# Kernel optimization log

Hardware: AMD Instinct MI355X
Metric: run time of the kernel (lower is better)

The kernel has to match this reference:

```python
import jax, jax.numpy as jnp
import numpy as np

B, S, D, H = 2, 2048, 1024, 16
HD = D // H  # 64
EPS = 1e-6


def setup_inputs() -> dict:
    key = jax.random.key(0)
    ks = jax.random.split(key, 12)
    s = 1.0 / np.sqrt(D)
    return {
        "query": jax.random.normal(ks[0], (B, S, D), jnp.float32),
        "key": jax.random.normal(ks[1], (B, S, D), jnp.float32),
        "value": jax.random.normal(ks[2], (B, S, D), jnp.float32),
        "mask": jax.random.randint(ks[3], (B, S, S), 0, 2) == 1,
        "Wq": jax.random.normal(ks[4], (D, D), jnp.float32) * s,
        "bq": jnp.zeros((D,), jnp.float32),
        "Wk": jax.random.normal(ks[5], (D, D), jnp.float32) * s,
        "bk": jnp.zeros((D,), jnp.float32),
        "Wv": jax.random.normal(ks[6], (D, D), jnp.float32) * s,
        "bv": jnp.zeros((D,), jnp.float32),
        "Wo": jax.random.normal(ks[7], (D, D), jnp.float32) * s,
        "bo": jnp.zeros((D,), jnp.float32),
        "gamma": jnp.ones((D,), jnp.float32),
        "beta": jnp.zeros((D,), jnp.float32),
    }


def reference(query, key, value, mask, Wq, bq, Wk, bk, Wv, bv, Wo, bo, gamma, beta):
    b, sq, _ = query.shape
    sk = key.shape[1]
    # QKV projections -> [b, h, s, hd]
    q = (query @ Wq + bq).reshape(b, sq, H, HD).transpose(0, 2, 1, 3)
    k = (key @ Wk + bk).reshape(b, sk, H, HD).transpose(0, 2, 1, 3)
    v = (value @ Wv + bv).reshape(b, sk, H, HD).transpose(0, 2, 1, 3)
    # scores [b, h, sq, sk]
    scores = jnp.einsum("bhqd,bhkd->bhqk", q, k) / jnp.sqrt(jnp.float32(HD))
    scores = jnp.where(mask[:, None, :, :], -jnp.inf, scores)
    attn = jax.nn.softmax(scores, axis=-1)  # dropout: eval mode (identity)
    out = jnp.einsum("bhqk,bhkd->bhqd", attn, v)
    out = out.transpose(0, 2, 1, 3).reshape(b, sq, H * HD)
    out = out @ Wo + bo
    # residual + LayerNorm with unbiased std and (std + eps) denominator (faithful to torch code)
    x = query + out
    mean = x.mean(-1, keepdims=True)
    std = jnp.std(x, axis=-1, keepdims=True, ddof=1)
    return gamma * (x - mean) / (std + EPS) + beta
```

## Files before the change

### kernel.cpp

```cpp
#include <hip/hip_runtime.h>


#define NB 2
#define SS 2048
#define DDIM 1024
#define NH 16
#define HDIM 64
#define MROWS (NB * SS)

typedef unsigned short u16;
typedef unsigned long long u64;
typedef unsigned int u32;
typedef short bf16x8 __attribute__((ext_vector_type(8)));
typedef float f32x4 __attribute__((ext_vector_type(4)));

typedef const __attribute__((address_space(1))) void GASV;
typedef __attribute__((address_space(3))) void LASV;

__device__ __forceinline__ float dev_exp2(float x) {
  float r;
  asm("v_exp_f32 %0, %1" : "=v"(r) : "v"(x));
  return r;
}

__device__ __forceinline__ u16 f2bf(float f) {
  unsigned u = __builtin_bit_cast(unsigned, f);
  u += 0x7FFFu + ((u >> 16) & 1u);
  return (u16)(u >> 16);
}

__device__ __forceinline__ u32 cvt_pk_bf16(float a, float b) {
  u32 d;
  asm("v_cvt_pk_bf16_f32 %0, %1, %2" : "=v"(d) : "v"(a), "v"(b));
  return d;
}

__global__ __launch_bounds__(256) void cvt_bf16_3(const float* __restrict__ q,
                                                  const float* __restrict__ k,
                                                  const float* __restrict__ v,
                                                  u16* __restrict__ out) {
  const float* in = (blockIdx.y == 0) ? q : (blockIdx.y == 1) ? k : v;
  size_t i = ((size_t)blockIdx.x * 256 + threadIdx.x) * 4;
  float4 val = *(const float4*)(in + i);
  uint2 o;
  u16* po = (u16*)&o;
  po[0] = f2bf(val.x); po[1] = f2bf(val.y); po[2] = f2bf(val.z); po[3] = f2bf(val.w);
  *(uint2*)(out + (size_t)blockIdx.y * MROWS * DDIM + i) = o;
}

__global__ __launch_bounds__(256) void cvt_mask_bits(const int* __restrict__ in,
                                                     u64* __restrict__ out) {
  size_t w = ((size_t)blockIdx.x * 256 + threadIdx.x) >> 6;
  int lane = threadIdx.x & 63;
  int v = in[w * 64 + lane];
  u64 bits = __ballot(v != 0);
  if (lane == 0) out[w] = bits;
}

__global__ __launch_bounds__(256) void transpose_cvt_w4(const float* __restrict__ W0,
                                                        const float* __restrict__ W1,
                                                        const float* __restrict__ W2,
                                                        const float* __restrict__ W3,
                                                        u16* __restrict__ WTbase) {
  __shared__ u16 t[64][65];
  const int z = blockIdx.z;
  const float* W = (z == 0) ? W0 : (z == 1) ? W1 : (z == 2) ? W2 : W3;
  u16* WT = WTbase + (size_t)z * DDIM * DDIM;
  const int k0 = blockIdx.x * 64, n0 = blockIdx.y * 64;
  const int tid = threadIdx.x;
  const int r = tid >> 4;
  const int c4 = (tid & 15) * 4;
#pragma unroll
  for (int it = 0; it < 4; ++it) {
    int k = r + it * 16;
    float4 v = *(const float4*)&W[(size_t)(k0 + k) * DDIM + n0 + c4];
    t[c4 + 0][k] = f2bf(v.x);
    t[c4 + 1][k] = f2bf(v.y);
    t[c4 + 2][k] = f2bf(v.z);
    t[c4 + 3][k] = f2bf(v.w);
  }
  __syncthreads();
#pragma unroll
  for (int it = 0; it < 4; ++it) {
    int n = r + it * 16;
    uint2 o;
    u16* po = (u16*)&o;
#pragma unroll
    for (int j = 0; j < 4; ++j) po[j] = t[n][c4 + j];
    *(uint2*)&WT[(size_t)(n0 + n) * DDIM + k0 + c4] = o;
  }
}

template <int MODE>
__global__ __launch_bounds__(256) void gemm_bt(const u16* __restrict__ Abase,
                                               const u16* __restrict__ BT,
                                               const float* __restrict__ b0,
                                               const float* __restrict__ b1,
                                               const float* __restrict__ b2,
                                               const float* __restrict__ resid,
                                               void* __restrict__ C,
                                               void* __restrict__ Cv) {
  __shared__ __align__(16) u16 SMEM[2][2][128][64];
  u16(&Al)[2][128][64] = SMEM[0];
  u16(&Bl)[2][128][64] = SMEM[1];
  const int tid = threadIdx.x;
  const int wid = tid >> 6, lane = tid & 63;
  const int wm = (wid >> 1) * 64, wn = (wid & 1) * 64;
  const int nwg = gridDim.x * gridDim.y;
  const int lin = blockIdx.y * 32 + blockIdx.x;
  const int wg = (lin & 7) * (nwg >> 3) + (lin >> 3);
  const int rowA0 = (wg & 31) * 128, colB0 = (wg >> 5) * 128;
  const int sel = (MODE == 0) ? (colB0 >> 10) : 0;
  const u16* Ag = Abase + (size_t)sel * ((size_t)MROWS * DDIM) + (size_t)rowA0 * DDIM;
  const u16* Bg = BT + (size_t)colB0 * DDIM;
  f32x4 acc[4][4] = {};
  const int rl = lane >> 3;
  const int ce = (lane & 7) * 8;

#define G_STAGE(buf, kt)                                                       \
  do {                                                                         \
    _Pragma("unroll") for (int c = 0; c < 4; ++c) {                            \
      int rt = wid * 32 + c * 8;                                               \
      __builtin_amdgcn_global_load_lds(                                        \
          (GASV*)(Ag + (size_t)(rt + rl) * DDIM + (kt) + ce),                  \
          (LASV*)((char*)&Al[buf][0][0] + rt * 128), 16, 0, 0);                \
      __builtin_amdgcn_global_load_lds(                                        \
          (GASV*)(Bg + (size_t)(rt + rl) * DDIM + (kt) + ce),                  \
          (LASV*)((char*)&Bl[buf][0][0] + rt * 128), 16, 0, 0);                \
    }                                                                          \
  } while (0)

  G_STAGE(0, 0);
  __syncthreads();
  for (int t = 0; t < 16; ++t) {
    const int cur = t & 1;
    if (t < 15) G_STAGE(cur ^ 1, (t + 1) * 64);
#pragma unroll
    for (int kk = 0; kk < 64; kk += 32) {
      bf16x8 af[4], bfr[4];
#pragma unroll
      for (int i = 0; i < 4; ++i)
        af[i] = *(const bf16x8*)&Al[cur][wm + i * 16 + (lane & 15)][kk + (lane >> 4) * 8];
#pragma unroll
      for (int j = 0; j < 4; ++j)
        bfr[j] = *(const bf16x8*)&Bl[cur][wn + j * 16 + (lane & 15)][kk + (lane >> 4) * 8];
#pragma unroll
      for (int i = 0; i < 4; ++i)
#pragma unroll
        for (int j = 0; j < 4; ++j)
          acc[i][j] = __builtin_amdgcn_mfma_f32_16x16x32_bf16(af[i], bfr[j], acc[i][j], 0, 0, 0);
    }
    __syncthreads();
  }
#undef G_STAGE

  const int cb = lane & 15, hi = lane >> 4;
  if (MODE == 0) {
    if (sel == 2) {
      u16(*T)[136] = (u16(*)[136]) & SMEM[0][0][0][0];
      const int dcol0 = colB0 & 1023;
#pragma unroll
      for (int j = 0; j < 4; ++j) {
        int dl = wn + j * 16 + cb;
        float bv = b2[dcol0 + dl];
#pragma unroll
        for (int i = 0; i < 4; ++i) {
          int sl = wm + i * 16 + hi * 4;
          uint2 o;
          o.x = cvt_pk_bf16(acc[i][j][0] + bv, acc[i][j][1] + bv);
          o.y = cvt_pk_bf16(acc[i][j][2] + bv, acc[i][j][3] + bv);
          *(uint2*)&T[dl][sl] = o;
        }
      }
      __syncthreads();
      const int bb = rowA0 >> 11, s0 = rowA0 & (SS - 1);
#pragma unroll
      for (int it = 0; it < 8; ++it) {
        int chunk = it * 256 + tid;
        int dl = chunk >> 4;
        int sc = (chunk & 15) * 8;
        int dg = dcol0 + dl;
        *(bf16x8*)&((u16*)Cv)[((size_t)(bb * NH + (dg >> 6)) * HDIM + (dg & 63)) * SS +
                              s0 + sc] = *(const bf16x8*)&T[dl][sc];
      }
    } else {
      const float* bp = (sel == 0) ? b0 : b1;
      const float scale = (sel == 0) ? 0.125f * 1.44269504088896340736f : 1.0f;
      u16* dst = (u16*)C + (size_t)sel * ((size_t)MROWS * DDIM);
      const int colw0 = (colB0 & 1023) + wn;
#pragma unroll
      for (int i = 0; i < 4; ++i)
#pragma unroll
        for (int j = 0; j < 4; ++j) {
          int colw = colw0 + j * 16 + cb;
          float bv = bp[colw];
#pragma unroll
          for (int r = 0; r < 4; ++r) {
            int row = rowA0 + wm + i * 16 + hi * 4 + r;
            dst[(size_t)row * DDIM + colw] = f2bf((acc[i][j][r] + bv) * scale);
          }
        }
    }
  } else {
#pragma unroll
    for (int i = 0; i < 4; ++i)
#pragma unroll
      for (int j = 0; j < 4; ++j) {
        int col = colB0 + wn + j * 16 + cb;
        float bv = b0[col];
#pragma unroll
        for (int r = 0; r < 4; ++r) {
          int row = rowA0 + wm + i * 16 + hi * 4 + r;
          size_t off = (size_t)row * DDIM + col;
          ((float*)C)[off] = acc[i][j][r] + bv + resid[off];
        }
      }
  }
}

__global__ __launch_bounds__(256, 4) void attn_fwd(const u16* __restrict__ Qp,
                                                   const u16* __restrict__ Kp,
                                                   const u16* __restrict__ VpT,
                                                   const u64* __restrict__ Mbits,
                                                   u16* __restrict__ O) {
  __shared__ __align__(16) u16 Kl[2][64][64];
  __shared__ __align__(16) u16 Vl[2][64][64];
  __shared__ __align__(16) u16 Pl[4][16][64];
  const int tid = threadIdx.x, wid = tid >> 6, lane = tid & 63;
  const int bid = blockIdx.x;
  const int bh = (bid & 7) * 4 + ((bid >> 3) & 3);
  const int q0 = (bid >> 5) * 64;
  const int b = bh >> 4, h = bh & 15;
  const int hi = lane >> 4, cbase = lane & 15, lx = lane & 7;

  bf16x8 qf[2];
  {
    const u16* qb = Qp + (size_t)(b * SS + q0 + wid * 16 + cbase) * DDIM + h * 64 + hi * 8;
    qf[0] = *(const bf16x8*)qb;
    qf[1] = *(const bf16x8*)(qb + 32);
  }
  float l_run = 0.f;
  f32x4 accO[4];
#pragma unroll
  for (int f = 0; f < 4; ++f) accO[f] = (f32x4){0.f, 0.f, 0.f, 0.f};

  const u16* Kgb = Kp + (size_t)b * SS * DDIM + h * 64;
  const u16* Vgb = VpT + (size_t)bh * 64 * SS;
  const u64* Mb = Mbits + (size_t)(b * SS + q0 + wid * 16 + cbase) * (SS / 64);
  const int rl = lane >> 3;
  const int ceS = ((lane & 7) ^ rl) * 8;

  int fo[4][2];
#pragma unroll
  for (int f = 0; f < 4; ++f)
#pragma unroll
    for (int ks = 0; ks < 2; ++ks)
      fo[f][ks] = (f * 16 + cbase) * 64 + (((ks * 4 + hi) ^ lx) << 3);
  int pw[4];
#pragma unroll
  for (int f = 0; f < 4; ++f)
    pw[f] = cbase * 64 + (((f * 2 + (hi >> 1)) ^ lx) << 3) + ((hi & 1) << 2);
  u16* KlF = &Kl[0][0][0];
  u16* VlF = &Vl[0][0][0];
  u16* Plw = &Pl[wid][0][0];

#define STAGE_KV(BUF, kv)                                                      \
  do {                                                                         \
    _Pragma("unroll") for (int c = 0; c < 2; ++c) {                            \
      int rt = wid * 16 + c * 8;                                               \
      __builtin_amdgcn_global_load_lds(                                        \
          (GASV*)(Kgb + (size_t)((kv) + rt + rl) * DDIM + ceS),                \
          (LASV*)((char*)KlF + (BUF) * 8192 + rt * 128), 16, 0, 0);            \
      __builtin_amdgcn_global_load_lds(                                        \
          (GASV*)(Vgb + (size_t)(rt + rl) * SS + (kv) + ceS),                  \
          (LASV*)((char*)VlF + (BUF) * 8192 + rt * 128), 16, 0, 0);            \
    }                                                                          \
  } while (0)

#define ATTN_ITER(T, CUR, DO_STAGE, MROW)                                      \
  do {                                                                         \
    if (DO_STAGE) STAGE_KV((CUR) ^ 1, ((T) + 1) * 64);                         \
    f32x4 sc[4];                                                               \
    __builtin_amdgcn_s_setprio(1);                                             \
    _Pragma("unroll") for (int fn = 0; fn < 4; ++fn) {                         \
      f32x4 c = (f32x4){0.f, 0.f, 0.f, 0.f};                                   \
      _Pragma("unroll") for (int ks = 0; ks < 2; ++ks) {                       \
        bf16x8 kf = *(const bf16x8*)(KlF + (CUR) * 4096 + fo[fn][ks]);         \
        c = __builtin_amdgcn_mfma_f32_16x16x32_bf16(kf, qf[ks], c, 0, 0, 0);   \
      }                                                                        \
      sc[fn] = c;                                                              \
    }                                                                          \
    __builtin_amdgcn_s_setprio(0);                                             \
             \
    u64 mh = (MROW) >> (hi * 4);                                               \
    u32 mlo = (u32)mh, mhi2 = (u32)(mh >> 32);                                 \
    float rs0 = 0.f, rs1 = 0.f;                                                \
    _Pragma("unroll") for (int fn = 0; fn < 4; ++fn) {                         \
      u32 b4 = ((fn < 2) ? mlo : mhi2) >> ((fn & 1) * 16);                     \
      _Pragma("unroll") for (int j = 0; j < 4; ++j) {                          \
        float bf_ = (float)((b4 >> j) & 1u);                                   \
        float p = dev_exp2(fmaf(bf_, -512.f, sc[fn][j]));                      \
        sc[fn][j] = p;                                                         \
        if (j & 1) rs1 += p; else rs0 += p;                                    \
      }                                                                        \
    }                                                                          \
    float rsum = rs0 + rs1;                                                    \
    rsum += __shfl_xor(rsum, 16, 64);                                          \
    rsum += __shfl_xor(rsum, 32, 64);                                          \
    l_run += rsum;                                                             \
    _Pragma("unroll") for (int fn = 0; fn < 4; ++fn) {                         \
      uint2 wpair;                                                             \
      wpair.x = cvt_pk_bf16(sc[fn][0], sc[fn][1]);                             \
      wpair.y = cvt_pk_bf16(sc[fn][2], sc[fn][3]);                             \
      *(uint2*)(Plw + pw[fn]) = wpair;                                         \
    }                                                                          \
    bf16x8 pf0 = *(const bf16x8*)(Plw + fo[0][0]);                             \
    bf16x8 pf1 = *(const bf16x8*)(Plw + fo[0][1]);                             \
    __builtin_amdgcn_s_setprio(1);                                             \
    _Pragma("unroll") for (int nd = 0; nd < 4; ++nd) {                         \
      bf16x8 v0 = *(const bf16x8*)(VlF + (CUR) * 4096 + fo[nd][0]);            \
      bf16x8 v1 = *(const bf16x8*)(VlF + (CUR) * 4096 + fo[nd][1]);            \
      accO[nd] = __builtin_amdgcn_mfma_f32_16x16x32_bf16(pf0, v0, accO[nd], 0, 0, 0); \
      accO[nd] = __builtin_amdgcn_mfma_f32_16x16x32_bf16(pf1, v1, accO[nd], 0, 0, 0); \
    }                                                                          \
    __builtin_amdgcn_s_setprio(0);                                             \
    __syncthreads();                                                           \
  } while (0)

  STAGE_KV(0, 0);
  __syncthreads();
  for (int th = 0; th < 16; ++th) {
    uint4 mw = *(const uint4*)&Mb[2 * th];
    u64 m0 = ((u64)mw.y << 32) | mw.x;
    u64 m1 = ((u64)mw.w << 32) | mw.z;
    ATTN_ITER(2 * th, 0, true, m0);
    ATTN_ITER(2 * th + 1, 1, (th != 15), m1);
  }
#undef ATTN_ITER
#undef STAGE_KV

  float lb[4];
#pragma unroll
  for (int j = 0; j < 4; ++j)
    lb[j] = __shfl(l_run, (lane & 48) + hi * 4 + j, 64);
#pragma unroll
  for (int nd = 0; nd < 4; ++nd)
#pragma unroll
    for (int j = 0; j < 4; ++j) {
      int row = q0 + wid * 16 + hi * 4 + j;
      int col = h * 64 + nd * 16 + cbase;
      O[(size_t)(b * SS + row) * DDIM + col] = f2bf(accO[nd][j] / lb[j]);
    }
}

__global__ __launch_bounds__(256) void ln_res(const float* __restrict__ xin,
                                              const float* __restrict__ gamma,
                                              const float* __restrict__ beta,
                                              float* __restrict__ out) {
  const int row = blockIdx.x, tid = threadIdx.x;
  const size_t base = (size_t)row * DDIM + tid * 4;
  float4 x = *(const float4*)(xin + base);
  float x0 = x.x, x1 = x.y, x2 = x.z, x3 = x.w;
  float s = x0 + x1 + x2 + x3;
  __shared__ float red[4];
#pragma unroll
  for (int off = 32; off >= 1; off >>= 1) s += __shfl_xor(s, off, 64);
  const int wid = tid >> 6, lane = tid & 63;
  if (lane == 0) red[wid] = s;
  __syncthreads();
  float mean = (red[0] + red[1] + red[2] + red[3]) * (1.0f / DDIM);
  float d0 = x0 - mean, d1 = x1 - mean, d2 = x2 - mean, d3 = x3 - mean;
  float ss = d0 * d0 + d1 * d1 + d2 * d2 + d3 * d3;
#pragma unroll
  for (int off = 32; off >= 1; off >>= 1) ss += __shfl_xor(ss, off, 64);
  __syncthreads();
  if (lane == 0) red[wid] = ss;
  __syncthreads();
  float var = (red[0] + red[1] + red[2] + red[3]) * (1.0f / (DDIM - 1));
  float denom = sqrtf(var) + 1e-6f;
  float4 g = *(const float4*)(gamma + (size_t)tid * 4);
  float4 be = *(const float4*)(beta + (size_t)tid * 4);
  float4 o;
  o.x = g.x * d0 / denom + be.x;
  o.y = g.y * d1 / denom + be.y;
  o.z = g.z * d2 / denom + be.z;
  o.w = g.w * d3 / denom + be.w;
  *(float4*)(out + base) = o;
}

extern "C" void kernel_launch(void* const* d_in, const int* in_sizes, int n_in,
                              void* d_out, int out_size, void* d_ws, size_t ws_size,
                              hipStream_t stream) {
  const float* query = (const float*)d_in[0];
  const float* key = (const float*)d_in[1];
  const float* value = (const float*)d_in[2];
  const int* mask = (const int*)d_in[3];
  const float* Wq = (const float*)d_in[4];
  const float* bq = (const float*)d_in[5];
  const float* Wk = (const float*)d_in[6];
  const float* bk = (const float*)d_in[7];
  const float* Wv = (const float*)d_in[8];
  const float* bv = (const float*)d_in[9];
  const float* Wo = (const float*)d_in[10];
  const float* bo = (const float*)d_in[11];
  const float* gamma = (const float*)d_in[12];
  const float* beta = (const float*)d_in[13];
  float* out = (float*)d_out;
  char* ws = (char*)d_ws;
  const size_t MB = 1ull << 20;
  u16* qkvb = (u16*)(ws + 0 * MB);
  u16* WT = (u16*)(ws + 24 * MB);
  u16* WoT = (u16*)(ws + 30 * MB);
  u16* Qp = (u16*)(ws + 32 * MB);
  u16* Kp = (u16*)(ws + 40 * MB);
  u16* VpT = (u16*)(ws + 48 * MB);
  u16* attnb = (u16*)(ws + 56 * MB);
  u64* maskbits = (u64*)(ws + 0 * MB);
  float* proj = (float*)(ws + 8 * MB);

  cvt_bf16_3<<<dim3(MROWS * DDIM / 1024, 3), 256, 0, stream>>>(query, key, value, qkvb);
  transpose_cvt_w4<<<dim3(16, 16, 4), 256, 0, stream>>>(Wq, Wk, Wv, Wo, WT);
  gemm_bt<0><<<dim3(32, 24), 256, 0, stream>>>(qkvb, WT, bq, bk, bv, nullptr, Qp, VpT);
  cvt_mask_bits<<<(NB * SS * SS) / 256, 256, 0, stream>>>(mask, maskbits);
  attn_fwd<<<1024, 256, 0, stream>>>(Qp, Kp, VpT, maskbits, attnb);
  gemm_bt<1><<<dim3(32, 8), 256, 0, stream>>>(attnb, WoT, bo, nullptr, nullptr,
                                              query, proj, nullptr);
  ln_res<<<MROWS, 256, 0, stream>>>(proj, gamma, beta, out);
}
```

Before: 161.5 us.

## Compute softmax row sums with MFMA and single-buffer GEMM LDS staging

In the attention kernel the per-iteration scalar row-sum of the probabilities and its cross-lane shuffles are replaced by two extra MFMAs that multiply the bf16 P tile by a ones vector. This also makes the normaliser match the rounded bf16 P values actually used in P·V. Separately, the projection GEMM drops its LDS double buffering for a single buffer that is loaded and then synchronised before compute each k-step, shrinking LDS use. That likely improves occupancy but exposes global-load latency that was previously overlapped.

```diff
diff --git a/kernel.cpp b/kernel.cpp
--- a/kernel.cpp
+++ b/kernel.cpp
@@ -100,9 +100,9 @@
                                                const float* __restrict__ resid,
                                                void* __restrict__ C,
                                                void* __restrict__ Cv) {
-  __shared__ __align__(16) u16 SMEM[2][2][128][64];
-  u16(&Al)[2][128][64] = SMEM[0];
-  u16(&Bl)[2][128][64] = SMEM[1];
+  __shared__ __align__(16) char SMEMRAW[34816];
+  u16(*Al)[64] = (u16(*)[64])SMEMRAW;
+  u16(*Bl)[64] = (u16(*)[64])(SMEMRAW + 16384);
   const int tid = threadIdx.x;
   const int wid = tid >> 6, lane = tid & 63;
   const int wm = (wid >> 1) * 64, wn = (wid & 1) * 64;
@@ -117,33 +117,31 @@
   const int rl = lane >> 3;
   const int ce = (lane & 7) * 8;
 
-#define G_STAGE(buf, kt)                                                       \
+#define G_STAGE(kt)                                                            \
   do {                                                                         \
     _Pragma("unroll") for (int c = 0; c < 4; ++c) {                            \
       int rt = wid * 32 + c * 8;                                               \
       __builtin_amdgcn_global_load_lds(                                        \
           (GASV*)(Ag + (size_t)(rt + rl) * DDIM + (kt) + ce),                  \
-          (LASV*)((char*)&Al[buf][0][0] + rt * 128), 16, 0, 0);                \
+          (LASV*)((char*)Al + rt * 128), 16, 0, 0);                            \
       __builtin_amdgcn_global_load_lds(                                        \
           (GASV*)(Bg + (size_t)(rt + rl) * DDIM + (kt) + ce),                  \
-          (LASV*)((char*)&Bl[buf][0][0] + rt * 128), 16, 0, 0);                \
+          (LASV*)((char*)Bl + rt * 128), 16, 0, 0);                            \
     }                                                                          \
   } while (0)
 
-  G_STAGE(0, 0);
-  __syncthreads();
   for (int t = 0; t < 16; ++t) {
-    const int cur = t & 1;
-    if (t < 15) G_STAGE(cur ^ 1, (t + 1) * 64);
+    G_STAGE(t * 64);
+    __syncthreads();
 #pragma unroll
     for (int kk = 0; kk < 64; kk += 32) {
       bf16x8 af[4], bfr[4];
 #pragma unroll
       for (int i = 0; i < 4; ++i)
-        af[i] = *(const bf16x8*)&Al[cur][wm + i * 16 + (lane & 15)][kk + (lane >> 4) * 8];
+        af[i] = *(const bf16x8*)&Al[wm + i * 16 + (lane & 15)][kk + (lane >> 4) * 8];
 #pragma unroll
       for (int j = 0; j < 4; ++j)
-        bfr[j] = *(const bf16x8*)&Bl[cur][wn + j * 16 + (lane & 15)][kk + (lane >> 4) * 8];
+        bfr[j] = *(const bf16x8*)&Bl[wn + j * 16 + (lane & 15)][kk + (lane >> 4) * 8];
 #pragma unroll
       for (int i = 0; i < 4; ++i)
 #pragma unroll
@@ -157,7 +155,7 @@
   const int cb = lane & 15, hi = lane >> 4;
   if (MODE == 0) {
     if (sel == 2) {
-      u16(*T)[136] = (u16(*)[136]) & SMEM[0][0][0][0];
+      u16(*T)[136] = (u16(*)[136])SMEMRAW;
       const int dcol0 = colB0 & 1023;
 #pragma unroll
       for (int j = 0; j < 4; ++j) {
@@ -239,7 +237,9 @@
     qf[0] = *(const bf16x8*)qb;
     qf[1] = *(const bf16x8*)(qb + 32);
   }
-  float l_run = 0.f;
+  const bf16x8 ONES8 = {(short)0x3F80, (short)0x3F80, (short)0x3F80, (short)0x3F80,
+                        (short)0x3F80, (short)0x3F80, (short)0x3F80, (short)0x3F80};
+  f32x4 l_acc = (f32x4){0.f, 0.f, 0.f, 0.f};
   f32x4 accO[4];
 #pragma unroll
   for (int f = 0; f < 4; ++f) accO[f] = (f32x4){0.f, 0.f, 0.f, 0.f};
@@ -294,20 +294,13 @@
              \
     u64 mh = (MROW) >> (hi * 4);                                               \
     u32 mlo = (u32)mh, mhi2 = (u32)(mh >> 32);                                 \
-    float rs0 = 0.f, rs1 = 0.f;                                                \
     _Pragma("unroll") for (int fn = 0; fn < 4; ++fn) {                         \
       u32 b4 = ((fn < 2) ? mlo : mhi2) >> ((fn & 1) * 16);                     \
       _Pragma("unroll") for (int j = 0; j < 4; ++j) {                          \
         float bf_ = (float)((b4 >> j) & 1u);                                   \
-        float p = dev_exp2(fmaf(bf_, -512.f, sc[fn][j]));                      \
-        sc[fn][j] = p;                                                         \
-        if (j & 1) rs1 += p; else rs0 += p;                                    \
+        sc[fn][j] = dev_exp2(fmaf(bf_, -512.f, sc[fn][j]));                    \
       }                                                                        \
     }                                                                          \
-    float rsum = rs0 + rs1;                                                    \
-    rsum += __shfl_xor(rsum, 16, 64);                                          \
-    rsum += __shfl_xor(rsum, 32, 64);                                          \
-    l_run += rsum;                                                             \
     _Pragma("unroll") for (int fn = 0; fn < 4; ++fn) {                         \
       uint2 wpair;                                                             \
       wpair.x = cvt_pk_bf16(sc[fn][0], sc[fn][1]);                             \
@@ -317,6 +310,8 @@
     bf16x8 pf0 = *(const bf16x8*)(Plw + fo[0][0]);                             \
     bf16x8 pf1 = *(const bf16x8*)(Plw + fo[0][1]);                             \
     __builtin_amdgcn_s_setprio(1);                                             \
+    l_acc = __builtin_amdgcn_mfma_f32_16x16x32_bf16(pf0, ONES8, l_acc, 0, 0, 0); \
+    l_acc = __builtin_amdgcn_mfma_f32_16x16x32_bf16(pf1, ONES8, l_acc, 0, 0, 0); \
     _Pragma("unroll") for (int nd = 0; nd < 4; ++nd) {                         \
       bf16x8 v0 = *(const bf16x8*)(VlF + (CUR) * 4096 + fo[nd][0]);            \
       bf16x8 v1 = *(const bf16x8*)(VlF + (CUR) * 4096 + fo[nd][1]);            \
@@ -339,17 +334,13 @@
 #undef ATTN_ITER
 #undef STAGE_KV
 
-  float lb[4];
-#pragma unroll
-  for (int j = 0; j < 4; ++j)
-    lb[j] = __shfl(l_run, (lane & 48) + hi * 4 + j, 64);
 #pragma unroll
   for (int nd = 0; nd < 4; ++nd)
 #pragma unroll
     for (int j = 0; j < 4; ++j) {
       int row = q0 + wid * 16 + hi * 4 + j;
       int col = h * 64 + nd * 16 + cbase;
-      O[(size_t)(b * SS + row) * DDIM + col] = f2bf(accO[nd][j] / lb[j]);
+      O[(size_t)(b * SS + row) * DDIM + col] = f2bf(accO[nd][j] / l_acc[j]);
     }
 }
 
```

New measurement: 176.0 us. 9.0% more time.
